# Kernel tuning notes

Hardware: AMD Instinct MI355X
Metric: run time of the kernel (lower is better)

Reference implementation:

```python
import jax, jax.numpy as jnp
import numpy as np

B, T = 64, 512
IN, OUT, H = 256, 256, 1024


def _lstm_cell(x, h, c, Wih, Whh, bih, bhh):
    # PyTorch LSTMCell: gates = x@Wih^T + bih + h@Whh^T + bhh, order i,f,g,o
    gates = x @ Wih.T + bih + h @ Whh.T + bhh
    i, f, g, o = jnp.split(gates, 4, axis=-1)
    c_new = jax.nn.sigmoid(f) * c + jax.nn.sigmoid(i) * jnp.tanh(g)
    h_new = jax.nn.sigmoid(o) * jnp.tanh(c_new)
    return h_new, c_new


def setup_inputs() -> dict:
    key = jax.random.key(0)
    ks = jax.random.split(key, 12)
    s = 1.0 / np.sqrt(H)  # torch default uniform(-1/sqrt(H), 1/sqrt(H))
    u = lambda k, shp: jax.random.uniform(k, shp, jnp.float32, -s, s)
    return {
        "z": jax.random.normal(ks[0], (B, H), jnp.float32),
        "x": jax.random.normal(ks[1], (B, T, IN), jnp.float32),
        "Wih0": u(ks[2], (4 * H, IN)),
        "Whh0": u(ks[3], (4 * H, H)),
        "bih0": u(ks[4], (4 * H,)),
        "bhh0": u(ks[5], (4 * H,)),
        "Wih1": u(ks[6], (4 * H, H)),
        "Whh1": u(ks[7], (4 * H, H)),
        "bih1": u(ks[8], (4 * H,)),
        "bhh1": u(ks[9], (4 * H,)),
        "Wlin": u(ks[10], (OUT, H)),
        "blin": u(ks[11], (OUT,)),
    }


def reference(z, x, Wih0, Whh0, bih0, bhh0, Wih1, Whh1, bih1, bhh1, Wlin, blin):
    # Teacher-forcing unroll: h_t[l] init to z, c_t[l] init to 0, first input is zeros,
    # then input at step t+1 is x[:, t].
    x_tb = jnp.swapaxes(x, 0, 1)  # [T, B, IN]
    c0_init = jnp.zeros_like(z)

    def step(carry, x_t):
        cur_in, h0, c0, h1, c1 = carry
        h0, c0 = _lstm_cell(cur_in, h0, c0, Wih0, Whh0, bih0, bhh0)
        h1, c1 = _lstm_cell(h0, h1, c1, Wih1, Whh1, bih1, bhh1)
        out_t = h1 @ Wlin.T + blin  # [B, OUT]
        return (x_t, h0, c0, h1, c1), out_t

    init = (jnp.zeros((z.shape[0], Wih0.shape[1]), z.dtype), z, c0_init, z, c0_init)
    _, outs = jax.lax.scan(step, init, x_tb)  # outs: [T, B, OUT]
    return jnp.swapaxes(outs, 0, 1)  # [B, T, OUT]
```

## Files before the change

kernel.cpp:

```cpp
#include <hip/hip_runtime.h>
#include <hip/hip_bf16.h>
#include <math.h>


typedef __attribute__((ext_vector_type(8))) short bf16x8;
typedef __attribute__((ext_vector_type(4))) float f32x4;
typedef unsigned long long u64;

__device__ __forceinline__ float sigm(float v) {
  return 1.f / (1.f + __expf(-v));
}
__device__ __forceinline__ float ftanh(float v) {
  return 2.f / (1.f + __expf(-2.f * v)) - 1.f;
}

__device__ __forceinline__ unsigned short bf16_bits(float v) {
  __hip_bfloat16 hb = __float2bfloat16(v);
  unsigned short us;
  __builtin_memcpy(&us, &hb, 2);
  return us;
}

__device__ __forceinline__ void vstore_bf16(__hip_bfloat16* p, float v) {
  *(volatile unsigned short*)p = bf16_bits(v);
}


__global__ __launch_bounds__(256) void prep_w0(const float* __restrict__ Wih0,
                                               const float* __restrict__ Whh0,
                                               __hip_bfloat16* __restrict__ W0) {
  const unsigned n = 4096u * 1280u;
  for (unsigned d = blockIdx.x * blockDim.x + threadIdx.x; d < n;
       d += blockDim.x * gridDim.x) {
    unsigned r = d / 1280u;
    unsigned k = d - r * 1280u;
    unsigned u = r >> 2, g = r & 3u;
    unsigned srow = g * 1024u + u;
    float v = (k < 256u) ? Wih0[(size_t)srow * 256u + k]
                         : Whh0[(size_t)srow * 1024u + (k - 256u)];
    W0[d] = __float2bfloat16(v);
  }
}

__global__ __launch_bounds__(256) void prep_w1(const float* __restrict__ Wih1,
                                               const float* __restrict__ Whh1,
                                               const float* __restrict__ Wlin,
                                               __hip_bfloat16* __restrict__ W1) {
  const unsigned n = 4352u * 2048u;
  for (unsigned d = blockIdx.x * blockDim.x + threadIdx.x; d < n;
       d += blockDim.x * gridDim.x) {
    unsigned r = d >> 11;
    unsigned k = d & 2047u;
    float v;
    if (r < 4096u) {
      unsigned u = r >> 2, g = r & 3u;
      unsigned srow = g * 1024u + u;
      v = (k < 1024u) ? Wih1[(size_t)srow * 1024u + k]
                      : Whh1[(size_t)srow * 1024u + (k - 1024u)];
    } else {
      unsigned o = r - 4096u;
      v = (k < 1024u) ? 0.f : Wlin[(size_t)o * 1024u + (k - 1024u)];
    }
    W1[d] = __float2bfloat16(v);
  }
}

__global__ __launch_bounds__(256) void prep_x(const float* __restrict__ x,
                                              __hip_bfloat16* __restrict__ xbf) {
  const unsigned n = 512u * 64u * 256u;
  for (unsigned d = blockIdx.x * blockDim.x + threadIdx.x; d < n;
       d += blockDim.x * gridDim.x) {
    unsigned t = d >> 14;
    unsigned b = (d >> 8) & 63u;
    unsigned k = d & 255u;
    float v = (t == 0u) ? 0.f : x[((size_t)b * 512u + (t - 1u)) * 256u + k];
    xbf[d] = __float2bfloat16(v);
  }
}

__global__ __launch_bounds__(256) void prep_misc(
    const float* __restrict__ bih0, const float* __restrict__ bhh0,
    const float* __restrict__ bih1, const float* __restrict__ bhh1,
    const float* __restrict__ z, float* __restrict__ b0, float* __restrict__ b1,
    __hip_bfloat16* __restrict__ h0buf, __hip_bfloat16* __restrict__ h1buf) {
  for (int i = blockIdx.x * blockDim.x + threadIdx.x; i < 73728;
       i += blockDim.x * gridDim.x) {
    if (i < 4096) {
      int u = i >> 2, g = i & 3;
      b0[i] = bih0[g * 1024 + u] + bhh0[g * 1024 + u];
    } else if (i < 8192) {
      int r = i - 4096;
      int u = r >> 2, g = r & 3;
      b1[r] = bih1[g * 1024 + u] + bhh1[g * 1024 + u];
    } else {
      int j = i - 8192;
      float zv = z[j];
      vstore_bf16(h0buf + j, zv);
      vstore_bf16(h1buf + 2 * 65536 + j, zv);
    }
  }
}


__device__ __forceinline__ void do_proj(const __hip_bfloat16* __restrict__ h1p,
                                        const bf16x8* wp, float (*red)[16][68],
                                        const float* __restrict__ blin,
                                        float* __restrict__ out, int pcol,
                                        int pbat, int t_out, int tid, int w,
                                        int col, int kq) {
  f32x4 a0 = {0.f, 0.f, 0.f, 0.f};
  const __hip_bfloat16* ab =
      h1p + ((size_t)((pbat << 4) + col) << 10) + (w << 7) + (kq << 3);
#pragma unroll
  for (int c = 0; c < 4; ++c) {
    bf16x8 f = *(const bf16x8*)(ab + (c << 5));
    a0 = __builtin_amdgcn_mfma_f32_16x16x32_bf16(f, wp[c], a0, 0, 0, 0);
  }
  *(f32x4*)&red[w][col][(kq << 2)] = a0;
  __syncthreads();
  if (tid < 256) {
    int o_l = tid & 15, b = tid >> 4;
    float v = blin[(pcol << 4) + o_l];
#pragma unroll
    for (int ww = 0; ww < 8; ++ww) v += red[ww][o_l][b];
    out[(((size_t)((pbat << 4) + b) << 9) + (size_t)t_out) * 256 + (pcol << 4) +
        o_l] = v;
  }
}


__global__ __launch_bounds__(512) void k_persist(
    const __hip_bfloat16* __restrict__ xbf, const __hip_bfloat16* __restrict__ W0,
    const __hip_bfloat16* __restrict__ W1, const float* __restrict__ b0,
    const float* __restrict__ b1, const float* __restrict__ blin,
    __hip_bfloat16* __restrict__ h0buf, __hip_bfloat16* __restrict__ h1buf,
    float* __restrict__ out, unsigned* __restrict__ flags) {
  const int tid = threadIdx.x;
  const int lane = tid & 63;
  const int w = tid >> 6;
  const int ks = w >> 1;
  const int ch = w & 1;
  const int bid = blockIdx.x;
  const int col = lane & 15;
  const int kq = lane >> 4;
  const bool isX = (bid < 128);
  const bool isproj = (bid >= 64 && bid < 128);
  const int pcol = bid & 15;
  const int pbat = (bid >> 4) & 3;

  __shared__ int s_agg, s_xcd;
  {
    unsigned* lead = flags + 256;
    if (tid == 0) {
      unsigned xcc = 0;
      asm volatile("s_getreg_b32 %0, hwreg(HW_REG_XCC_ID)" : "=s"(xcc));
      xcc &= 7u;
      unsigned old = __hip_atomic_fetch_add(&lead[xcc], 1u, __ATOMIC_RELAXED,
                                            __HIP_MEMORY_SCOPE_AGENT);
      s_agg = (old == 0u) ? 1 : 0;
      s_xcd = (int)xcc;
    }
  }

  bf16x8 wa[10], wb[16], wp[4];
  if (isX) {
    const int gcol = (bid << 5) + (ch << 4) + col;
    const __hip_bfloat16* p = W0 + (size_t)gcol * 1280 + ks * 320 + (kq << 3);
#pragma unroll
    for (int c = 0; c < 10; ++c) wa[c] = *(const bf16x8*)(p + (c << 5));
    if (isproj) {
      const __hip_bfloat16* q = W1 +
          ((size_t)(4096 + (pcol << 4) + col) << 11) + 1024 + (w << 7) +
          (kq << 3);
#pragma unroll
      for (int c = 0; c < 4; ++c) wp[c] = *(const bf16x8*)(q + (c << 5));
    } else {
#pragma unroll
      for (int c = 0; c < 4; ++c) wp[c] = bf16x8{0, 0, 0, 0, 0, 0, 0, 0};
    }
  } else {
    const int gcol = ((bid - 128) << 5) + (ch << 4) + col;
    const __hip_bfloat16* p = W1 + ((size_t)gcol << 11) + (ks << 9) + (kq << 3);
#pragma unroll
    for (int c = 0; c < 16; ++c) wb[c] = *(const bf16x8*)(p + (c << 5));
  }

  const int u_l = tid & 7, bq = tid >> 3;
  const int ubase = (isX ? (bid << 3) : ((bid - 128) << 3));
  float bias[4];
  {
    const float* bsrc = isX ? b0 : b1;
#pragma unroll
    for (int g = 0; g < 4; ++g) bias[g] = bsrc[((ubase + u_l) << 2) + g];
  }
  float cv = 0.f;

  __shared__ float red[4][32][68];

  __syncthreads();

  unsigned* rel = flags + 272 + (s_xcd << 4);

  for (int k = 0; k <= 512; ++k) {
    if (isX) {
      if (k < 512) {
        const __hip_bfloat16* h0prev = h0buf + ((size_t)(k & 1) << 16);
        f32x4 a0 = {0.f, 0.f, 0.f, 0.f}, a1 = a0, a2 = a0, a3 = a0;
#pragma unroll
        for (int c = 0; c < 10; ++c) {
          const int k0 = ks * 320 + (c << 5);
          const __hip_bfloat16* ab;
          size_t rs;
          if (k0 < 256) {
            ab = xbf + ((size_t)k << 14) + k0 + (kq << 3);
            rs = 256;
          } else {
            ab = h0prev + (k0 - 256) + (kq << 3);
            rs = 1024;
          }
          bf16x8 f0 = *(const bf16x8*)(ab + (size_t)col * rs);
          bf16x8 f1 = *(const bf16x8*)(ab + (size_t)(16 + col) * rs);
          bf16x8 f2 = *(const bf16x8*)(ab + (size_t)(32 + col) * rs);
          bf16x8 f3 = *(const bf16x8*)(ab + (size_t)(48 + col) * rs);
          a0 = __builtin_amdgcn_mfma_f32_16x16x32_bf16(f0, wa[c], a0, 0, 0, 0);
          a1 = __builtin_amdgcn_mfma_f32_16x16x32_bf16(f1, wa[c], a1, 0, 0, 0);
          a2 = __builtin_amdgcn_mfma_f32_16x16x32_bf16(f2, wa[c], a2, 0, 0, 0);
          a3 = __builtin_amdgcn_mfma_f32_16x16x32_bf16(f3, wa[c], a3, 0, 0, 0);
        }
        const int rc = (ch << 4) + col;
        *(f32x4*)&red[ks][rc][(kq << 2)] = a0;
        *(f32x4*)&red[ks][rc][16 + (kq << 2)] = a1;
        *(f32x4*)&red[ks][rc][32 + (kq << 2)] = a2;
        *(f32x4*)&red[ks][rc][48 + (kq << 2)] = a3;
        __syncthreads();
        {
          float gg[4];
#pragma unroll
          for (int g = 0; g < 4; ++g) {
            float v = bias[g];
#pragma unroll
            for (int ww = 0; ww < 4; ++ww) v += red[ww][(u_l << 2) + g][bq];
            gg[g] = v;
          }
          float cn = sigm(gg[1]) * cv + sigm(gg[0]) * ftanh(gg[2]);
          cv = cn;
          vstore_bf16(h0buf + ((size_t)((k + 1) & 1) << 16) +
                          ((size_t)bq << 10) + ubase + u_l,
                      sigm(gg[3]) * ftanh(cn));
        }
        __syncthreads();
      }
      if (isproj && k >= 3)
        do_proj(h1buf + (((size_t)(k % 3)) << 16), wp,
                (float(*)[16][68])red, blin, out, pcol, pbat, k - 3, tid, w,
                col, kq);
    } else {
      if (k >= 1) {
        const __hip_bfloat16* h0cur = h0buf + ((size_t)(k & 1) << 16);
        const __hip_bfloat16* h1prev = h1buf + ((size_t)((k + 1) % 3) << 16);
        f32x4 a0 = {0.f, 0.f, 0.f, 0.f}, a1 = a0, a2 = a0, a3 = a0;
#pragma unroll
        for (int c = 0; c < 16; ++c) {
          const int k0 = (ks << 9) + (c << 5);
          const __hip_bfloat16* ab =
              ((k0 < 1024) ? h0cur + k0 : h1prev + (k0 - 1024)) + (kq << 3);
          bf16x8 f0 = *(const bf16x8*)(ab + ((size_t)col << 10));
          bf16x8 f1 = *(const bf16x8*)(ab + ((size_t)(16 + col) << 10));
          bf16x8 f2 = *(const bf16x8*)(ab + ((size_t)(32 + col) << 10));
          bf16x8 f3 = *(const bf16x8*)(ab + ((size_t)(48 + col) << 10));
          a0 = __builtin_amdgcn_mfma_f32_16x16x32_bf16(f0, wb[c], a0, 0, 0, 0);
          a1 = __builtin_amdgcn_mfma_f32_16x16x32_bf16(f1, wb[c], a1, 0, 0, 0);
          a2 = __builtin_amdgcn_mfma_f32_16x16x32_bf16(f2, wb[c], a2, 0, 0, 0);
          a3 = __builtin_amdgcn_mfma_f32_16x16x32_bf16(f3, wb[c], a3, 0, 0, 0);
        }
        const int rc = (ch << 4) + col;
        *(f32x4*)&red[ks][rc][(kq << 2)] = a0;
        *(f32x4*)&red[ks][rc][16 + (kq << 2)] = a1;
        *(f32x4*)&red[ks][rc][32 + (kq << 2)] = a2;
        *(f32x4*)&red[ks][rc][48 + (kq << 2)] = a3;
        __syncthreads();
        {
          float gg[4];
#pragma unroll
          for (int g = 0; g < 4; ++g) {
            float v = bias[g];
#pragma unroll
            for (int ww = 0; ww < 4; ++ww) v += red[ww][(u_l << 2) + g][bq];
            gg[g] = v;
          }
          float cn = sigm(gg[1]) * cv + sigm(gg[0]) * ftanh(gg[2]);
          cv = cn;
          vstore_bf16(h1buf + ((size_t)((k + 2) % 3) << 16) +
                          ((size_t)bq << 10) + ubase + u_l,
                      sigm(gg[3]) * ftanh(cn));
        }
      }
    }

    __builtin_amdgcn_s_waitcnt(0);
    __syncthreads();
    if (tid == 0)
      __hip_atomic_store(&flags[bid], (unsigned)(k + 1), __ATOMIC_RELAXED,
                         __HIP_MEMORY_SCOPE_AGENT);
    if (w == 0) {
      const unsigned tgt = (unsigned)(k + 1);
      if (s_agg) {
        const u64* fq = (const u64*)flags;
        for (;;) {
          u64 q0 = __hip_atomic_load(&fq[2 * lane], __ATOMIC_RELAXED,
                                     __HIP_MEMORY_SCOPE_AGENT);
          u64 q1 = __hip_atomic_load(&fq[2 * lane + 1], __ATOMIC_RELAXED,
                                     __HIP_MEMORY_SCOPE_AGENT);
          int ok = ((unsigned)q0 >= tgt) & ((unsigned)(q0 >> 32) >= tgt) &
                   ((unsigned)q1 >= tgt) & ((unsigned)(q1 >> 32) >= tgt);
          if (__all(ok)) break;
          __builtin_amdgcn_s_sleep(1);
        }
        __builtin_amdgcn_fence(__ATOMIC_ACQUIRE, "agent");
        if (lane == 0)
          __hip_atomic_store(rel, tgt, __ATOMIC_RELAXED,
                             __HIP_MEMORY_SCOPE_AGENT);
      } else {
        while (__hip_atomic_load(rel, __ATOMIC_RELAXED,
                                 __HIP_MEMORY_SCOPE_AGENT) < tgt)
          __builtin_amdgcn_s_sleep(1);
        if (bid < 8) {
          __builtin_amdgcn_fence(__ATOMIC_ACQUIRE, "agent");
        } else {
          __builtin_amdgcn_sched_barrier(0);
          asm volatile("buffer_inv" ::: "memory");
          __builtin_amdgcn_sched_barrier(0);
        }
      }
    }
    __syncthreads();
  }

  if (isproj) {
    do_proj(h1buf, wp, (float(*)[16][68])red, blin, out, pcol, pbat, 510, tid,
            w, col, kq);
    __syncthreads();
    do_proj(h1buf + ((size_t)1 << 16), wp, (float(*)[16][68])red, blin, out,
            pcol, pbat, 511, tid, w, col, kq);
  }
}


extern "C" void kernel_launch(void* const* d_in, const int* in_sizes, int n_in,
                              void* d_out, int out_size, void* d_ws, size_t ws_size,
                              hipStream_t stream) {
  const float* z = (const float*)d_in[0];
  const float* x = (const float*)d_in[1];
  const float* Wih0 = (const float*)d_in[2];
  const float* Whh0 = (const float*)d_in[3];
  const float* bih0 = (const float*)d_in[4];
  const float* bhh0 = (const float*)d_in[5];
  const float* Wih1 = (const float*)d_in[6];
  const float* Whh1 = (const float*)d_in[7];
  const float* bih1 = (const float*)d_in[8];
  const float* bhh1 = (const float*)d_in[9];
  const float* Wlin = (const float*)d_in[10];
  const float* blin = (const float*)d_in[11];
  float* out = (float*)d_out;

  char* ws = (char*)d_ws;
  __hip_bfloat16* W0 = (__hip_bfloat16*)(ws);
  __hip_bfloat16* W1 = (__hip_bfloat16*)(ws + 10485760);
  __hip_bfloat16* xbf = (__hip_bfloat16*)(ws + 28311552);
  float* b0 = (float*)(ws + 45088768);
  float* b1 = (float*)(ws + 45105152);
  __hip_bfloat16* h0buf = (__hip_bfloat16*)(ws + 45121536);
  __hip_bfloat16* h1buf = (__hip_bfloat16*)(ws + 45383680);
  unsigned* flags = (unsigned*)(ws + 45776896);

  hipMemsetAsync(flags, 0, 4096, stream);
  prep_w0<<<4096, 256, 0, stream>>>(Wih0, Whh0, W0);
  prep_w1<<<4096, 256, 0, stream>>>(Wih1, Whh1, Wlin, W1);
  prep_x<<<4096, 256, 0, stream>>>(x, xbf);
  prep_misc<<<288, 256, 0, stream>>>(bih0, bhh0, bih1, bhh1, z, b0, b1, h0buf,
                                     h1buf);

  k_persist<<<256, 512, 0, stream>>>(xbf, W0, W1, b0, b1, blin, h0buf, h1buf,
                                     out, flags);
}
```

Baseline: 9.242 ms.

## Co-locate layer-0 and layer-1 gate tiles in each block with 8-deep h buffers

Each of the 256 blocks now computes 16 gate columns of both layers: four waves do the layer-1 matmul (previous h0 and h1) and four waves do the layer-0 matmul (x and h0), replacing the old split of 128 blocks per layer. h0 and h1 histories move to 8-slot ring buffers. The cache acquire/invalidate is now issued only every fourth step, and the projection runs one step earlier. The aim is to balance work across blocks and cut per-step synchronization and invalidation cost. The price is more register pressure, since every block holds 16 weight fragments, and a correctness risk if the deeper buffering and the relaxed invalidation cadence ever let stale h values be read.

```diff
diff --git a/kernel.cpp b/kernel.cpp
--- a/kernel.cpp
+++ b/kernel.cpp
@@ -95,8 +95,8 @@
     } else {
       int j = i - 8192;
       float zv = z[j];
-      vstore_bf16(h0buf + j, zv);
-      vstore_bf16(h1buf + 2 * 65536 + j, zv);
+      vstore_bf16(h0buf + 7 * 65536 + j, zv);
+      vstore_bf16(h1buf + 7 * 65536 + j, zv);
     }
   }
 }
@@ -138,12 +138,11 @@
   const int tid = threadIdx.x;
   const int lane = tid & 63;
   const int w = tid >> 6;
-  const int ks = w >> 1;
-  const int ch = w & 1;
   const int bid = blockIdx.x;
+  const int cb = bid << 4;
   const int col = lane & 15;
   const int kq = lane >> 4;
-  const bool isX = (bid < 128);
+  const int n = cb + col;
   const bool isproj = (bid >= 64 && bid < 128);
   const int pcol = bid & 15;
   const int pbat = (bid >> 4) & 3;
@@ -162,140 +161,150 @@
     }
   }
 
-  bf16x8 wa[10], wb[16], wp[4];
-  if (isX) {
-    const int gcol = (bid << 5) + (ch << 4) + col;
-    const __hip_bfloat16* p = W0 + (size_t)gcol * 1280 + ks * 320 + (kq << 3);
-#pragma unroll
-    for (int c = 0; c < 10; ++c) wa[c] = *(const bf16x8*)(p + (c << 5));
-    if (isproj) {
-      const __hip_bfloat16* q = W1 +
-          ((size_t)(4096 + (pcol << 4) + col) << 11) + 1024 + (w << 7) +
-          (kq << 3);
-#pragma unroll
-      for (int c = 0; c < 4; ++c) wp[c] = *(const bf16x8*)(q + (c << 5));
-    } else {
-#pragma unroll
-      for (int c = 0; c < 4; ++c) wp[c] = bf16x8{0, 0, 0, 0, 0, 0, 0, 0};
-    }
+  bf16x8 wreg[16], wp[4];
+  if (w < 4) {
+    const __hip_bfloat16* p = W1 + ((size_t)n << 11) + (w << 9) + (kq << 3);
+#pragma unroll
+    for (int c = 0; c < 16; ++c) wreg[c] = *(const bf16x8*)(p + (c << 5));
   } else {
-    const int gcol = ((bid - 128) << 5) + (ch << 4) + col;
-    const __hip_bfloat16* p = W1 + ((size_t)gcol << 11) + (ks << 9) + (kq << 3);
-#pragma unroll
-    for (int c = 0; c < 16; ++c) wb[c] = *(const bf16x8*)(p + (c << 5));
-  }
-
-  const int u_l = tid & 7, bq = tid >> 3;
-  const int ubase = (isX ? (bid << 3) : ((bid - 128) << 3));
+    const __hip_bfloat16* p = W0 + (size_t)n * 1280 + (w - 4) * 320 + (kq << 3);
+#pragma unroll
+    for (int c = 0; c < 10; ++c) wreg[c] = *(const bf16x8*)(p + (c << 5));
+#pragma unroll
+    for (int c = 10; c < 16; ++c) wreg[c] = bf16x8{0, 0, 0, 0, 0, 0, 0, 0};
+  }
+  if (isproj) {
+    const __hip_bfloat16* p = W1 +
+        ((size_t)(4096 + (pcol << 4) + col) << 11) + 1024 + (w << 7) + (kq << 3);
+#pragma unroll
+    for (int c = 0; c < 4; ++c) wp[c] = *(const bf16x8*)(p + (c << 5));
+  } else {
+#pragma unroll
+    for (int c = 0; c < 4; ++c) wp[c] = bf16x8{0, 0, 0, 0, 0, 0, 0, 0};
+  }
+
+  const int tc = tid & 255;
+  const int u_l = tc & 3, bq = tc >> 2;
+  const bool is0 = (tid < 256);
   float bias[4];
   {
-    const float* bsrc = isX ? b0 : b1;
-#pragma unroll
-    for (int g = 0; g < 4; ++g) bias[g] = bsrc[((ubase + u_l) << 2) + g];
+    const float* bsrc = is0 ? b0 : b1;
+#pragma unroll
+    for (int g = 0; g < 4; ++g) bias[g] = bsrc[cb + (u_l << 2) + g];
   }
   float cv = 0.f;
 
-  __shared__ float red[4][32][68];
+  __shared__ float red[8][16][68];
 
   __syncthreads();
 
   unsigned* rel = flags + 272 + (s_xcd << 4);
 
   for (int k = 0; k <= 512; ++k) {
-    if (isX) {
+    const __hip_bfloat16* h0p = h0buf + ((size_t)((k + 7) & 7) << 16);
+    const __hip_bfloat16* h1pp = h1buf + ((size_t)((k + 6) & 7) << 16);
+
+    if (w < 4) {
+      if (k >= 1) {
+        f32x4 a0 = {0.f, 0.f, 0.f, 0.f}, a1 = a0, a2 = a0, a3 = a0;
+#pragma unroll
+        for (int c = 0; c < 16; ++c) {
+          const int k0 = (w << 9) + (c << 5);
+          const __hip_bfloat16* ab =
+              ((k0 < 1024) ? h0p + k0 : h1pp + (k0 - 1024)) + (kq << 3);
+          bf16x8 f0 = *(const bf16x8*)(ab + ((size_t)col << 10));
+          bf16x8 f1 = *(const bf16x8*)(ab + ((size_t)(16 + col) << 10));
+          bf16x8 f2 = *(const bf16x8*)(ab + ((size_t)(32 + col) << 10));
+          bf16x8 f3 = *(const bf16x8*)(ab + ((size_t)(48 + col) << 10));
+          a0 = __builtin_amdgcn_mfma_f32_16x16x32_bf16(f0, wreg[c], a0, 0, 0, 0);
+          a1 = __builtin_amdgcn_mfma_f32_16x16x32_bf16(f1, wreg[c], a1, 0, 0, 0);
+          a2 = __builtin_amdgcn_mfma_f32_16x16x32_bf16(f2, wreg[c], a2, 0, 0, 0);
+          a3 = __builtin_amdgcn_mfma_f32_16x16x32_bf16(f3, wreg[c], a3, 0, 0, 0);
+        }
+        *(f32x4*)&red[w][col][(kq << 2)] = a0;
+        *(f32x4*)&red[w][col][16 + (kq << 2)] = a1;
+        *(f32x4*)&red[w][col][32 + (kq << 2)] = a2;
+        *(f32x4*)&red[w][col][48 + (kq << 2)] = a3;
+      }
+    } else {
       if (k < 512) {
-        const __hip_bfloat16* h0prev = h0buf + ((size_t)(k & 1) << 16);
         f32x4 a0 = {0.f, 0.f, 0.f, 0.f}, a1 = a0, a2 = a0, a3 = a0;
 #pragma unroll
         for (int c = 0; c < 10; ++c) {
-          const int k0 = ks * 320 + (c << 5);
+          const int k0 = (w - 4) * 320 + (c << 5);
           const __hip_bfloat16* ab;
           size_t rs;
           if (k0 < 256) {
             ab = xbf + ((size_t)k << 14) + k0 + (kq << 3);
             rs = 256;
           } else {
-            ab = h0prev + (k0 - 256) + (kq << 3);
+            ab = h0p + (k0 - 256) + (kq << 3);
             rs = 1024;
           }
           bf16x8 f0 = *(const bf16x8*)(ab + (size_t)col * rs);
           bf16x8 f1 = *(const bf16x8*)(ab + (size_t)(16 + col) * rs);
           bf16x8 f2 = *(const bf16x8*)(ab + (size_t)(32 + col) * rs);
           bf16x8 f3 = *(const bf16x8*)(ab + (size_t)(48 + col) * rs);
-          a0 = __builtin_amdgcn_mfma_f32_16x16x32_bf16(f0, wa[c], a0, 0, 0, 0);
-          a1 = __builtin_amdgcn_mfma_f32_16x16x32_bf16(f1, wa[c], a1, 0, 0, 0);
-          a2 = __builtin_amdgcn_mfma_f32_16x16x32_bf16(f2, wa[c], a2, 0, 0, 0);
-          a3 = __builtin_amdgcn_mfma_f32_16x16x32_bf16(f3, wa[c], a3, 0, 0, 0);
-        }
-        const int rc = (ch << 4) + col;
-        *(f32x4*)&red[ks][rc][(kq << 2)] = a0;
-        *(f32x4*)&red[ks][rc][16 + (kq << 2)] = a1;
-        *(f32x4*)&red[ks][rc][32 + (kq << 2)] = a2;
-        *(f32x4*)&red[ks][rc][48 + (kq << 2)] = a3;
-        __syncthreads();
-        {
-          float gg[4];
-#pragma unroll
-          for (int g = 0; g < 4; ++g) {
-            float v = bias[g];
-#pragma unroll
-            for (int ww = 0; ww < 4; ++ww) v += red[ww][(u_l << 2) + g][bq];
-            gg[g] = v;
-          }
-          float cn = sigm(gg[1]) * cv + sigm(gg[0]) * ftanh(gg[2]);
-          cv = cn;
-          vstore_bf16(h0buf + ((size_t)((k + 1) & 1) << 16) +
-                          ((size_t)bq << 10) + ubase + u_l,
-                      sigm(gg[3]) * ftanh(cn));
-        }
-        __syncthreads();
-      }
-      if (isproj && k >= 3)
-        do_proj(h1buf + (((size_t)(k % 3)) << 16), wp,
-                (float(*)[16][68])red, blin, out, pcol, pbat, k - 3, tid, w,
-                col, kq);
+          a0 = __builtin_amdgcn_mfma_f32_16x16x32_bf16(f0, wreg[c], a0, 0, 0, 0);
+          a1 = __builtin_amdgcn_mfma_f32_16x16x32_bf16(f1, wreg[c], a1, 0, 0, 0);
+          a2 = __builtin_amdgcn_mfma_f32_16x16x32_bf16(f2, wreg[c], a2, 0, 0, 0);
+          a3 = __builtin_amdgcn_mfma_f32_16x16x32_bf16(f3, wreg[c], a3, 0, 0, 0);
+        }
+        *(f32x4*)&red[w][col][(kq << 2)] = a0;
+        *(f32x4*)&red[w][col][16 + (kq << 2)] = a1;
+        *(f32x4*)&red[w][col][32 + (kq << 2)] = a2;
+        *(f32x4*)&red[w][col][48 + (kq << 2)] = a3;
+      }
+    }
+    __syncthreads();
+
+    if (is0) {
+      if (k < 512) {
+        float gg[4];
+#pragma unroll
+        for (int g = 0; g < 4; ++g) {
+          float v = bias[g];
+#pragma unroll
+          for (int ww = 0; ww < 4; ++ww) v += red[4 + ww][(u_l << 2) + g][bq];
+          gg[g] = v;
+        }
+        float cn = sigm(gg[1]) * cv + sigm(gg[0]) * ftanh(gg[2]);
+        cv = cn;
+        vstore_bf16(h0buf + ((size_t)(k & 7) << 16) + ((size_t)bq << 10) +
+                        (cb >> 2) + u_l,
+                    sigm(gg[3]) * ftanh(cn));
+      }
     } else {
       if (k >= 1) {
-        const __hip_bfloat16* h0cur = h0buf + ((size_t)(k & 1) << 16);
-        const __hip_bfloat16* h1prev = h1buf + ((size_t)((k + 1) % 3) << 16);
-        f32x4 a0 = {0.f, 0.f, 0.f, 0.f}, a1 = a0, a2 = a0, a3 = a0;
-#pragma unroll
-        for (int c = 0; c < 16; ++c) {
-          const int k0 = (ks << 9) + (c << 5);
-          const __hip_bfloat16* ab =
-              ((k0 < 1024) ? h0cur + k0 : h1prev + (k0 - 1024)) + (kq << 3);
-          bf16x8 f0 = *(const bf16x8*)(ab + ((size_t)col << 10));
-          bf16x8 f1 = *(const bf16x8*)(ab + ((size_t)(16 + col) << 10));
-          bf16x8 f2 = *(const bf16x8*)(ab + ((size_t)(32 + col) << 10));
-          bf16x8 f3 = *(const bf16x8*)(ab + ((size_t)(48 + col) << 10));
-          a0 = __builtin_amdgcn_mfma_f32_16x16x32_bf16(f0, wb[c], a0, 0, 0, 0);
-          a1 = __builtin_amdgcn_mfma_f32_16x16x32_bf16(f1, wb[c], a1, 0, 0, 0);
-          a2 = __builtin_amdgcn_mfma_f32_16x16x32_bf16(f2, wb[c], a2, 0, 0, 0);
-          a3 = __builtin_amdgcn_mfma_f32_16x16x32_bf16(f3, wb[c], a3, 0, 0, 0);
-        }
-        const int rc = (ch << 4) + col;
-        *(f32x4*)&red[ks][rc][(kq << 2)] = a0;
-        *(f32x4*)&red[ks][rc][16 + (kq << 2)] = a1;
-        *(f32x4*)&red[ks][rc][32 + (kq << 2)] = a2;
-        *(f32x4*)&red[ks][rc][48 + (kq << 2)] = a3;
-        __syncthreads();
-        {
-          float gg[4];
-#pragma unroll
-          for (int g = 0; g < 4; ++g) {
-            float v = bias[g];
-#pragma unroll
-            for (int ww = 0; ww < 4; ++ww) v += red[ww][(u_l << 2) + g][bq];
-            gg[g] = v;
-          }
-          float cn = sigm(gg[1]) * cv + sigm(gg[0]) * ftanh(gg[2]);
-          cv = cn;
-          vstore_bf16(h1buf + ((size_t)((k + 2) % 3) << 16) +
-                          ((size_t)bq << 10) + ubase + u_l,
-                      sigm(gg[3]) * ftanh(cn));
-        }
-      }
-    }
+        float gg[4];
+#pragma unroll
+        for (int g = 0; g < 4; ++g) {
+          float v = bias[g];
+#pragma unroll
+          for (int ww = 0; ww < 4; ++ww) v += red[ww][(u_l << 2) + g][bq];
+          gg[g] = v;
+        }
+        float cn = sigm(gg[1]) * cv + sigm(gg[0]) * ftanh(gg[2]);
+        cv = cn;
+        vstore_bf16(h1buf + ((size_t)((k + 7) & 7) << 16) + ((size_t)bq << 10) +
+                        (cb >> 2) + u_l,
+                    sigm(gg[3]) * ftanh(cn));
+      }
+    }
+    __syncthreads();
+
+    if ((k & 3) == 0 && w == 0) {
+      __builtin_amdgcn_sched_barrier(0);
+      if (s_agg || bid >= 248) {
+        __builtin_amdgcn_fence(__ATOMIC_ACQUIRE, "agent");
+      } else {
+        asm volatile("buffer_inv" ::: "memory");
+      }
+      __builtin_amdgcn_sched_barrier(0);
+    }
+
+    if (isproj && k >= 2)
+      do_proj(h1pp, wp, red, blin, out, pcol, pbat, k - 2, tid, w, col, kq);
 
     __builtin_amdgcn_s_waitcnt(0);
     __syncthreads();
@@ -316,7 +325,6 @@
           if (__all(ok)) break;
           __builtin_amdgcn_s_sleep(1);
         }
-        __builtin_amdgcn_fence(__ATOMIC_ACQUIRE, "agent");
         if (lane == 0)
           __hip_atomic_store(rel, tgt, __ATOMIC_RELAXED,
                              __HIP_MEMORY_SCOPE_AGENT);
@@ -324,25 +332,17 @@
         while (__hip_atomic_load(rel, __ATOMIC_RELAXED,
                                  __HIP_MEMORY_SCOPE_AGENT) < tgt)
           __builtin_amdgcn_s_sleep(1);
-        if (bid < 8) {
-          __builtin_amdgcn_fence(__ATOMIC_ACQUIRE, "agent");
-        } else {
-          __builtin_amdgcn_sched_barrier(0);
-          asm volatile("buffer_inv" ::: "memory");
-          __builtin_amdgcn_sched_barrier(0);
-        }
       }
     }
     __syncthreads();
   }
 
-  if (isproj) {
-    do_proj(h1buf, wp, (float(*)[16][68])red, blin, out, pcol, pbat, 510, tid,
-            w, col, kq);
-    __syncthreads();
-    do_proj(h1buf + ((size_t)1 << 16), wp, (float(*)[16][68])red, blin, out,
-            pcol, pbat, 511, tid, w, col, kq);
-  }
+  if (!isproj) return;
+  if (w == 0)
+    __builtin_amdgcn_fence(__ATOMIC_ACQUIRE, "agent");
+  __syncthreads();
+  do_proj(h1buf + ((size_t)7 << 16), wp, red, blin, out, pcol, pbat, 511, tid,
+          w, col, kq);
 }
 
 
@@ -370,8 +370,8 @@
   float* b0 = (float*)(ws + 45088768);
   float* b1 = (float*)(ws + 45105152);
   __hip_bfloat16* h0buf = (__hip_bfloat16*)(ws + 45121536);
-  __hip_bfloat16* h1buf = (__hip_bfloat16*)(ws + 45383680);
-  unsigned* flags = (unsigned*)(ws + 45776896);
+  __hip_bfloat16* h1buf = (__hip_bfloat16*)(ws + 46170112);
+  unsigned* flags = (unsigned*)(ws + 47218688);
 
   hipMemsetAsync(flags, 0, 4096, stream);
   prep_w0<<<4096, 256, 0, stream>>>(Wih0, Whh0, W0);
```

Measured after the change: 8.632 ms. 1.07x faster.
